# Optimization experiments

Measured on AMD Instinct MI355X. Metric: run time of the kernel, lower is better.

Reference implementation:

```python
import jax, jax.numpy as jnp
import numpy as np

L, H, NH, HD, F, B, S = 32, 1024, 16, 64, 2048, 2, 2048
HPH = H // NH  # hidden per attention head (hyena column split)
EPS = 1e-6
BLOCK = {0:'HCS',4:'HCS',7:'HCS',11:'HCS',14:'HCS',18:'HCS',21:'HCS',25:'HCS',28:'HCS',
         1:'HCM',5:'HCM',8:'HCM',12:'HCM',15:'HCM',19:'HCM',22:'HCM',26:'HCM',29:'HCM',
         2:'HCL',6:'HCL',9:'HCL',13:'HCL',16:'HCL',20:'HCL',23:'HCL',27:'HCL',30:'HCL',
         3:'ATT',10:'ATT',17:'ATT',24:'ATT',31:'ATT'}

def rmsnorm(x, w):
    return x * jax.lax.rsqrt(jnp.mean(x * x, -1, keepdims=True) + EPS) * w

def step_fir(u, state, w, b, flip=False, gated=False):
    # u:[B,C]  state:[B,C,cache]  w:[C,Lf]  b:[C]  (single-token FIR step)
    cache = state.shape[-1]
    w = w[:, ::-1][:, -(cache + 1):] if flip else w[:, :cache + 1]
    y = w[:, -1] * u + jnp.sum(state * w[:, :-1], -1)
    y = y + (b * u if gated else b)
    return y

def split3(z):
    # column_split_hyena=True path of _interleave_split
    r = z.reshape(z.shape[0], NH, 3 * HPH)
    x2 = r[:, :, :HPH].reshape(z.shape[0], H)
    x1 = r[:, :, HPH:2 * HPH].reshape(z.shape[0], H)
    v = r[:, :, 2 * HPH:].reshape(z.shape[0], H)
    return x2, x1, v

def mlp(x, W1, W2):
    return jax.nn.gelu(x @ W1.T) @ W2.T

def fir_block(x, n1, n2, pW, pb, oW, ob, W1, W2, sfw, sfb, h, D, fstate, istate, flip, gated):
    xn = rmsnorm(x, n1)
    z = xn @ pW.T + pb                 # [B,1,3H]
    u = z[:, -1]                       # [B,3H]
    zp = step_fir(u, fstate, sfw, sfb)
    x2, x1, v = split3(zp)
    y = step_fir(x1 * v, istate, h, D, flip=flip, gated=gated)
    y = (y * x2)[:, None]              # [B,1,H]
    x = y @ oW.T + ob + x
    return mlp(rmsnorm(x, n2), W1, W2) + x

def hcl_block(x, n1, n2, pW, pb, oW, ob, W1, W2, sfw, sfb, log_poles, residues, D, fstate, iir):
    xn = rmsnorm(x, n1)
    z = xn @ pW.T + pb
    u = z[:, -1]
    zp = step_fir(u, fstate, sfw, sfb)
    x2, x1, v = split3(zp)
    x1v = x1 * v
    iir_new = jnp.exp(log_poles) * iir + x1v[..., None]   # [B,H,SS] single-step IIR update
    res = jnp.sum(residues * iir_new, -1)
    y = (x2 * (res + D * x1v))[:, None]
    x = y @ oW.T + ob + x
    return mlp(rmsnorm(x, n2), W1, W2) + x

def att_block(x, n1, n2, qW, qb, oW, ob, W1, W2, kc, vc, cos, sin, pos):
    xn = rmsnorm(x, n1)
    qkv = (xn @ qW.T + qb).reshape(B, 1, 3, NH, HD)
    q, k, v = qkv[:, :, 0], qkv[:, :, 1], qkv[:, :, 2]
    c = jnp.concatenate([cos[pos], cos[pos]])  # [HD]
    s = jnp.concatenate([sin[pos], sin[pos]])
    rot = lambda t: jnp.concatenate([-t[..., HD // 2:], t[..., :HD // 2]], -1)
    q = q * c + rot(q) * s
    k = k * c + rot(k) * s
    kc = kc.at[:, pos].set(k[:, 0])  # KV-cache scatter write at current position
    vc = vc.at[:, pos].set(v[:, 0])
    scores = jnp.einsum('bohd,bshd->bhos', q, kc) * (HD ** -0.5)
    scores = jnp.where(jnp.arange(S) > pos, -10000.0, scores)
    aw = jax.nn.softmax(scores, -1)
    ctx = jnp.einsum('bhos,bshd->bohd', aw, vc).reshape(B, 1, H)
    x = ctx @ oW.T + ob + x
    return mlp(rmsnorm(x, n2), W1, W2) + x

def forward(x, position, norm1_w, norm2_w, proj_W, proj_b, out_W, out_b, mlp_W1, mlp_W2,
            sf_w, sf_b, hcs_h, hcs_D, hcm_h, hcm_D, hcl_logpoles, hcl_residues, hcl_D,
            fir_state, hcs_state, hcm_state, iir_state, k_cache, v_cache, rope_cos, rope_sin):
    att = 0
    for i in range(L):  # loop over 32 structurally distinct layers (static)
        t = BLOCK[i]
        cm = (norm1_w[i], norm2_w[i], proj_W[i], proj_b[i], out_W[i], out_b[i], mlp_W1[i], mlp_W2[i])
        if t == 'HCS':
            x = fir_block(x, *cm, sf_w[i], sf_b[i], hcs_h[i], hcs_D[i], fir_state[i], hcs_state[i], False, False)
        elif t == 'HCM':
            x = fir_block(x, *cm, sf_w[i], sf_b[i], hcm_h[i], hcm_D[i], fir_state[i], hcm_state[i], True, True)
        elif t == 'HCL':
            x = hcl_block(x, *cm, sf_w[i], sf_b[i], hcl_logpoles[i], hcl_residues[i], hcl_D[i], fir_state[i], iir_state[i])
        else:
            x = att_block(x, *cm, k_cache[att], v_cache[att], rope_cos, rope_sin, position)
            att += 1
    return x

def setup_inputs():
    key = jax.random.key(0)
    ks = jax.random.split(key, 24)
    g = lambda k, shape, sc: jax.random.normal(k, shape, jnp.float32) * sc
    inv_freq = 1.0 / (10000.0 ** (np.arange(0, HD, 2, dtype=np.float32) / HD))
    ang = np.arange(S, dtype=np.float32)[:, None] * inv_freq[None, :]
    return {
        'x': g(ks[0], (B, 1, H), 1.0),
        'position': 1024,
        'norm1_w': jnp.ones((L, H), jnp.float32),
        'norm2_w': jnp.ones((L, H), jnp.float32),
        'proj_W': g(ks[1], (L, 3 * H, H), H ** -0.5),
        'proj_b': jnp.zeros((L, 3 * H), jnp.float32),
        'out_W': g(ks[2], (L, H, H), 0.2 * H ** -0.5),
        'out_b': jnp.zeros((L, H), jnp.float32),
        'mlp_W1': g(ks[3], (L, F, H), H ** -0.5),
        'mlp_W2': g(ks[4], (L, H, F), 0.2 * F ** -0.5),
        'sf_w': g(ks[5], (L, 3 * H, 3), 0.4),
        'sf_b': g(ks[6], (L, 3 * H), 0.02),
        'hcs_h': g(ks[7], (L, H, 7), 0.2),
        'hcs_D': g(ks[8], (L, H), 0.2),
        'hcm_h': g(ks[9], (L, H, 128), 0.04),
        'hcm_D': g(ks[10], (L, H), 0.2),
        'hcl_logpoles': -jax.random.uniform(ks[11], (L, H, 16), jnp.float32, 0.01, 2.0),
        'hcl_residues': g(ks[12], (L, H, 16), 0.1),
        'hcl_D': g(ks[13], (L, H), 0.2),
        'fir_state': g(ks[14], (L, B, 3 * H, 2), 0.5),
        'hcs_state': g(ks[15], (L, B, H, 6), 0.5),
        'hcm_state': g(ks[16], (L, B, H, 127), 0.5),
        'iir_state': g(ks[17], (L, B, H, 16), 0.5),
        'k_cache': g(ks[18], (5, B, S, NH, HD), 1.0),
        'v_cache': g(ks[19], (5, B, S, NH, HD), 1.0),
        'rope_cos': jnp.asarray(np.cos(ang)),
        'rope_sin': jnp.asarray(np.sin(ang)),
    }

def reference(x, position, norm1_w, norm2_w, proj_W, proj_b, out_W, out_b, mlp_W1, mlp_W2,
              sf_w, sf_b, hcs_h, hcs_D, hcm_h, hcm_D, hcl_logpoles, hcl_residues, hcl_D,
              fir_state, hcs_state, hcm_state, iir_state, k_cache, v_cache, rope_cos, rope_sin):
    return forward(x, position, norm1_w, norm2_w, proj_W, proj_b, out_W, out_b, mlp_W1, mlp_W2,
                   sf_w, sf_b, hcs_h, hcs_D, hcm_h, hcm_D, hcl_logpoles, hcl_residues, hcl_D,
                   fir_state, hcs_state, hcm_state, iir_state, k_cache, v_cache, rope_cos, rope_sin)
```

## Files before the change

### kernel.cpp

```cpp
#include <hip/hip_runtime.h>
#include <hip/hip_bf16.h>
#include <math.h>

#define LAYERS 32
#define H      1024
#define H3     3072
#define NHEADS 16
#define HDIM   64
#define FF     2048
#define BATCH  2
#define SEQ    2048
#define EPSF   1e-6f

__device__ __forceinline__ float wredSum(float v) {
#pragma unroll
  for (int m = 32; m >= 1; m >>= 1) v += __shfl_xor(v, m, 64);
  return v;
}
__device__ __forceinline__ float wredMax(float v) {
#pragma unroll
  for (int m = 32; m >= 1; m >>= 1) v = fmaxf(v, __shfl_xor(v, m, 64));
  return v;
}
__device__ __forceinline__ float gelu_t(float x) {
  return 0.5f * x * (1.0f + tanhf(0.7978845608028654f * (x + 0.044715f * x * x * x)));
}

__global__ __launch_bounds__(256) void prep_kernel(
    const float* __restrict__ sf_w, const float* __restrict__ sf_b,
    const float* __restrict__ fir_state,
    const float* __restrict__ hcs_h, const float* __restrict__ hcs_D, const float* __restrict__ hcs_state,
    const float* __restrict__ hcm_h, const float* __restrict__ hcm_D, const float* __restrict__ hcm_state,
    const float* __restrict__ lp, const float* __restrict__ resd, const float* __restrict__ hcl_D,
    const float* __restrict__ iir,
    unsigned long long kbits,
    float* __restrict__ sfd, float* __restrict__ sfc,
    float* __restrict__ mix0, float* __restrict__ mix1)
{
  int blk = blockIdx.x, tid = threadIdx.x;
  if (blk < 768) {
    int idx = blk * 256 + tid;
    int i = idx / (BATCH * H3);
    int r = idx % (BATCH * H3);
    int b = r / H3, ch = r % H3;
    const float* fs = fir_state + ((size_t)(i * BATCH + b) * H3 + ch) * 2;
    const float* sw = sf_w + ((size_t)i * H3 + ch) * 3;
    sfd[idx] = fs[0] * sw[0] + fs[1] * sw[1] + sf_b[i * H3 + ch];
    if (b == 0) sfc[i * H3 + ch] = sw[2];
  } else if (blk < 1024) {
    int idx = (blk - 768) * 256 + tid;
    int i = idx >> 11;
    int r = idx & 2047;
    int b = r >> 10, c = r & 1023;
    int kind = (int)((kbits >> (2 * i)) & 3ull);
    if (kind == 0) {
      const float* st = hcs_state + ((size_t)(i * BATCH + b) * H + c) * 6;
      const float* hh = hcs_h + ((size_t)i * H + c) * 7;
      float acc = 0.f;
#pragma unroll
      for (int k = 0; k < 6; k++) acc += st[k] * hh[k];
      mix0[idx] = acc + hcs_D[i * H + c];
      if (b == 0) mix1[i * H + c] = hh[6];
    } else if (kind == 2) {
      const float* ii = iir + ((size_t)(i * BATCH + b) * H + c) * 16;
      const float* lpp = lp + ((size_t)i * H + c) * 16;
      const float* rs = resd + ((size_t)i * H + c) * 16;
      float acc = 0.f, rsum = 0.f;
#pragma unroll
      for (int k = 0; k < 16; k++) { float rv = rs[k]; acc += rv * expf(lpp[k]) * ii[k]; rsum += rv; }
      mix0[idx] = acc;
      if (b == 0) mix1[i * H + c] = rsum + hcl_D[i * H + c];
    }
  } else {
    int w = tid >> 6, lane = tid & 63;
    int widx = (blk - 1024) * 4 + w;
    if (widx < 9 * BATCH * H) {
      int li = widx >> 11;
      int r = widx & 2047;
      int b = r >> 10, c = r & 1023;
      int i = (li >> 1) * 7 + ((li & 1) ? 5 : 1);
      const float* st = hcm_state + ((size_t)(i * BATCH + b) * H + c) * 127;
      const float* hh = hcm_h + ((size_t)i * H + c) * 128;
      float acc = 0.f;
      int k = lane;
      if (k < 127) acc += st[k] * hh[127 - k];
      k = lane + 64;
      if (k < 127) acc += st[k] * hh[127 - k];
      acc = wredSum(acc);
      if (lane == 0) {
        mix0[(i * BATCH + b) * H + c] = acc;
        if (b == 0) mix1[i * H + c] = hh[0] + hcm_D[i * H + c];
      }
    }
  }
}

template<int ROWS, bool GELU, bool HASBIAS>
__global__ __launch_bounds__(256) void gemv_norm_kernel(
    const float* __restrict__ x, const float* __restrict__ nw,
    const float* __restrict__ W, const float* __restrict__ bias,
    float* __restrict__ out)
{
  __shared__ alignas(16) float xe[BATCH][H];
  __shared__ float red[8];
  __shared__ float scl[BATCH];
  int tid = threadIdx.x, lane = tid & 63, w = tid >> 6;
  int r0 = blockIdx.x * 8 + w * 2;
  const float4* row0 = (const float4*)(W + (size_t)r0 * H);
  const float4* row1 = (const float4*)(W + (size_t)(r0 + 1) * H);
  float4 wa[4], wb[4];
#pragma unroll
  for (int j = 0; j < 4; j++) { wa[j] = row0[lane + 64 * j]; wb[j] = row1[lane + 64 * j]; }

  float ss0 = 0.f, ss1 = 0.f;
#pragma unroll
  for (int it = 0; it < 8; it++) {
    int e = tid + it * 256;
    int b = e >> 10, c = e & 1023;
    float xv = x[b * H + c];
    xe[b][c] = xv * nw[c];
    if (it < 4) ss0 += xv * xv; else ss1 += xv * xv;
  }
  ss0 = wredSum(ss0); ss1 = wredSum(ss1);
  if (lane == 0) { red[w] = ss0; red[4 + w] = ss1; }
  __syncthreads();
  if (tid == 0) {
    scl[0] = rsqrtf((red[0] + red[1] + red[2] + red[3]) * (1.0f / H) + EPSF);
    scl[1] = rsqrtf((red[4] + red[5] + red[6] + red[7]) * (1.0f / H) + EPSF);
  }
  __syncthreads();

  float a00 = 0.f, a01 = 0.f, a10 = 0.f, a11 = 0.f;
  const float4* x0 = (const float4*)xe[0];
  const float4* x1 = (const float4*)xe[1];
#pragma unroll
  for (int j = 0; j < 4; j++) {
    float4 h0 = x0[lane + 64 * j], h1 = x1[lane + 64 * j];
    a00 += wa[j].x * h0.x + wa[j].y * h0.y + wa[j].z * h0.z + wa[j].w * h0.w;
    a01 += wa[j].x * h1.x + wa[j].y * h1.y + wa[j].z * h1.z + wa[j].w * h1.w;
    a10 += wb[j].x * h0.x + wb[j].y * h0.y + wb[j].z * h0.z + wb[j].w * h0.w;
    a11 += wb[j].x * h1.x + wb[j].y * h1.y + wb[j].z * h1.z + wb[j].w * h1.w;
  }
  a00 = wredSum(a00); a01 = wredSum(a01); a10 = wredSum(a10); a11 = wredSum(a11);
  if (lane == 0) {
    float s0 = scl[0], s1 = scl[1];
    float b0 = HASBIAS ? bias[r0] : 0.f;
    float b1 = HASBIAS ? bias[r0 + 1] : 0.f;
    float v00 = a00 * s0 + b0, v01 = a01 * s1 + b0;
    float v10 = a10 * s0 + b1, v11 = a11 * s1 + b1;
    if (GELU) { v00 = gelu_t(v00); v01 = gelu_t(v01); v10 = gelu_t(v10); v11 = gelu_t(v11); }
    out[0 * ROWS + r0] = v00;
    out[1 * ROWS + r0] = v01;
    out[0 * ROWS + r0 + 1] = v10;
    out[1 * ROWS + r0 + 1] = v11;
  }
}

__global__ __launch_bounds__(256) void mix_out_kernel(
    int kind,
    const float* __restrict__ z, const float* __restrict__ sfdL, const float* __restrict__ sfcL,
    const float* __restrict__ mix0L, const float* __restrict__ mix1L,
    const float* __restrict__ attP,
    const float* __restrict__ oW, const float* __restrict__ ob,
    const float* __restrict__ x_in, float* __restrict__ x_out)
{
  __shared__ alignas(16) float y[BATCH][H];
  int tid = threadIdx.x, lane = tid & 63, w = tid >> 6;
  int r0 = blockIdx.x * 8 + w * 2;
  const float4* row0 = (const float4*)(oW + (size_t)r0 * H);
  const float4* row1 = (const float4*)(oW + (size_t)(r0 + 1) * H);
  float4 wa[4], wb[4];
#pragma unroll
  for (int j = 0; j < 4; j++) { wa[j] = row0[lane + 64 * j]; wb[j] = row1[lane + 64 * j]; }

  if (kind < 3) {
#pragma unroll
    for (int it = 0; it < 8; it++) {
      int e = tid + it * 256;
      int b = e >> 10, c = e & 1023;
      int n = c >> 6, d = c & 63;
      int base = n * 192 + d;
      float x2 = sfcL[base] * z[b * H3 + base] + sfdL[b * H3 + base];
      float x1 = sfcL[base + 64] * z[b * H3 + base + 64] + sfdL[b * H3 + base + 64];
      float vv = sfcL[base + 128] * z[b * H3 + base + 128] + sfdL[b * H3 + base + 128];
      float t = x1 * vv;
      y[b][c] = (mix1L[c] * t + mix0L[b * H + c]) * x2;
    }
  } else {
#pragma unroll
    for (int it = 0; it < 8; it++) {
      int e = tid + it * 256;
      int b = e >> 10, c = e & 1023;
      int n = c >> 6, d = c & 63;
      float M = -1e30f;
#pragma unroll
      for (int sp = 0; sp < 8; sp++) M = fmaxf(M, attP[((sp * BATCH + b) * NHEADS + n) * 66 + 64]);
      float Ls = 0.f, num = 0.f;
#pragma unroll
      for (int sp = 0; sp < 8; sp++) {
        const float* P = attP + ((sp * BATCH + b) * NHEADS + n) * 66;
        float wgt = expf(P[64] - M);
        Ls += wgt * P[65];
        num += wgt * P[d];
      }
      y[b][c] = num / Ls;
    }
  }
  __syncthreads();

  float a00 = 0.f, a01 = 0.f, a10 = 0.f, a11 = 0.f;
  const float4* y0 = (const float4*)y[0];
  const float4* y1 = (const float4*)y[1];
#pragma unroll
  for (int j = 0; j < 4; j++) {
    float4 h0 = y0[lane + 64 * j], h1 = y1[lane + 64 * j];
    a00 += wa[j].x * h0.x + wa[j].y * h0.y + wa[j].z * h0.z + wa[j].w * h0.w;
    a01 += wa[j].x * h1.x + wa[j].y * h1.y + wa[j].z * h1.z + wa[j].w * h1.w;
    a10 += wb[j].x * h0.x + wb[j].y * h0.y + wb[j].z * h0.z + wb[j].w * h0.w;
    a11 += wb[j].x * h1.x + wb[j].y * h1.y + wb[j].z * h1.z + wb[j].w * h1.w;
  }
  a00 = wredSum(a00); a01 = wredSum(a01); a10 = wredSum(a10); a11 = wredSum(a11);
  if (lane == 0) {
    x_out[0 * H + r0]     = a00 + ob[r0]     + x_in[0 * H + r0];
    x_out[1 * H + r0]     = a01 + ob[r0]     + x_in[1 * H + r0];
    x_out[0 * H + r0 + 1] = a10 + ob[r0 + 1] + x_in[0 * H + r0 + 1];
    x_out[1 * H + r0 + 1] = a11 + ob[r0 + 1] + x_in[1 * H + r0 + 1];
  }
}

__global__ __launch_bounds__(256) void gemv_mlp2_kernel(
    const float* __restrict__ h, const float* __restrict__ W2,
    const float* __restrict__ x_in, float* __restrict__ x_out)
{
  __shared__ alignas(16) float hs[BATCH][FF];
  int tid = threadIdx.x, lane = tid & 63, w = tid >> 6;
  int r = blockIdx.x * 4 + w;
  const float4* row = (const float4*)(W2 + (size_t)r * FF);
  float4 wv[8];
#pragma unroll
  for (int j = 0; j < 8; j++) wv[j] = row[lane + 64 * j];
#pragma unroll
  for (int it = 0; it < 16; it++) {
    int e = tid + it * 256;
    int b = e >> 11, c = e & 2047;
    hs[b][c] = h[b * FF + c];
  }
  __syncthreads();
  float a0 = 0.f, a1 = 0.f;
  const float4* h0 = (const float4*)hs[0];
  const float4* h1 = (const float4*)hs[1];
#pragma unroll
  for (int j = 0; j < 8; j++) {
    float4 p = h0[lane + 64 * j], q = h1[lane + 64 * j];
    a0 += wv[j].x * p.x + wv[j].y * p.y + wv[j].z * p.z + wv[j].w * p.w;
    a1 += wv[j].x * q.x + wv[j].y * q.y + wv[j].z * q.z + wv[j].w * q.w;
  }
  a0 = wredSum(a0); a1 = wredSum(a1);
  if (lane == 0) {
    x_out[0 * H + r] = a0 + x_in[0 * H + r];
    x_out[1 * H + r] = a1 + x_in[1 * H + r];
  }
}

__global__ __launch_bounds__(256) void attn_kernel(
    const float* __restrict__ z, const int* __restrict__ posp,
    const float* __restrict__ kc, const float* __restrict__ vc,
    const float* __restrict__ cosT, const float* __restrict__ sinT,
    float* __restrict__ P)
{
  int sp = blockIdx.x & 7, n = (blockIdx.x >> 3) & 15, b = blockIdx.x >> 7;
  int pos = *posp;
  __shared__ alignas(16) float q_s[HDIM], k_s[HDIM], v_s[HDIM];
  __shared__ float eg[256];
  __shared__ float redA[4];
  __shared__ alignas(16) float osum[4][HDIM];
  int tid = threadIdx.x, lane = tid & 63, w = tid >> 6;

  if (tid < 64) {
    int d = tid, j = d & 31;
    float cs = cosT[pos * 32 + j], sn = sinT[pos * 32 + j];
    float qv = z[b * H3 + n * 64 + d];
    float qo = z[b * H3 + n * 64 + ((d + 32) & 63)];
    q_s[d] = ((d < 32) ? (qv * cs - qo * sn) : (qv * cs + qo * sn)) * 0.125f;
    float kv = z[b * H3 + 1024 + n * 64 + d];
    float ko = z[b * H3 + 1024 + n * 64 + ((d + 32) & 63)];
    k_s[d] = (d < 32) ? (kv * cs - ko * sn) : (kv * cs + ko * sn);
    v_s[d] = z[b * H3 + 2048 + n * 64 + d];
  }
  __syncthreads();

  int s = sp * 256 + tid;
  float logit = -1e30f;
  if (s <= pos) {
    const float4* k4 = (s == pos) ? (const float4*)k_s
                                  : (const float4*)(kc + (((size_t)b * SEQ + s) * NHEADS + n) * HDIM);
    const float4* q4 = (const float4*)q_s;
    float acc = 0.f;
#pragma unroll
    for (int j = 0; j < 16; j++) {
      float4 kk = k4[j], qq = q4[j];
      acc += kk.x * qq.x + kk.y * qq.y + kk.z * qq.z + kk.w * qq.w;
    }
    logit = acc;
  }
  float m = wredMax(logit);
  if (lane == 0) redA[w] = m;
  __syncthreads();
  m = fmaxf(fmaxf(redA[0], redA[1]), fmaxf(redA[2], redA[3]));
  float e = (s <= pos) ? expf(logit - m) : 0.f;
  eg[tid] = e;
  float ps = wredSum(e);
  __syncthreads();
  if (lane == 0) redA[w] = ps;
  __syncthreads();
  float lsum = redA[0] + redA[1] + redA[2] + redA[3];

  int dgrp = lane & 15, srow = lane >> 4;
  float4 acc = make_float4(0.f, 0.f, 0.f, 0.f);
#pragma unroll 4
  for (int it = 0; it < 16; it++) {
    int sl = w * 64 + it * 4;
    if (sp * 256 + sl > pos) break;
    int sli = sl + srow;
    int ss = sp * 256 + sli;
    float ev = eg[sli];
    const float4* v4 = (ss == pos) ? (const float4*)v_s
                                   : (const float4*)(vc + (((size_t)b * SEQ + ss) * NHEADS + n) * HDIM);
    float4 vv = v4[dgrp];
    acc.x += ev * vv.x; acc.y += ev * vv.y; acc.z += ev * vv.z; acc.w += ev * vv.w;
  }
#pragma unroll
  for (int mm = 16; mm <= 32; mm <<= 1) {
    acc.x += __shfl_xor(acc.x, mm, 64);
    acc.y += __shfl_xor(acc.y, mm, 64);
    acc.z += __shfl_xor(acc.z, mm, 64);
    acc.w += __shfl_xor(acc.w, mm, 64);
  }
  if (srow == 0) ((float4*)osum[w])[dgrp] = acc;
  __syncthreads();
  float* Pp = P + ((size_t)(sp * BATCH + b) * NHEADS + n) * 66;
  if (tid < 64) Pp[tid] = osum[0][tid] + osum[1][tid] + osum[2][tid] + osum[3][tid];
  if (tid == 64) Pp[64] = m;
  if (tid == 65) Pp[65] = lsum;
}

extern "C" void kernel_launch(void* const* d_in, const int* in_sizes, int n_in,
                              void* d_out, int out_size, void* d_ws, size_t ws_size,
                              hipStream_t stream) {
  (void)in_sizes; (void)n_in; (void)out_size; (void)ws_size;
  const float* x0    = (const float*)d_in[0];
  const int*   posp  = (const int*)d_in[1];
  const float* n1    = (const float*)d_in[2];
  const float* n2    = (const float*)d_in[3];
  const float* pW    = (const float*)d_in[4];
  const float* pb    = (const float*)d_in[5];
  const float* oW    = (const float*)d_in[6];
  const float* ob    = (const float*)d_in[7];
  const float* W1    = (const float*)d_in[8];
  const float* W2    = (const float*)d_in[9];
  const float* sfw   = (const float*)d_in[10];
  const float* sfb   = (const float*)d_in[11];
  const float* hcs_h = (const float*)d_in[12];
  const float* hcs_D = (const float*)d_in[13];
  const float* hcm_h = (const float*)d_in[14];
  const float* hcm_D = (const float*)d_in[15];
  const float* lp    = (const float*)d_in[16];
  const float* resd  = (const float*)d_in[17];
  const float* hclD  = (const float*)d_in[18];
  const float* fir   = (const float*)d_in[19];
  const float* hcsS  = (const float*)d_in[20];
  const float* hcmS  = (const float*)d_in[21];
  const float* iir   = (const float*)d_in[22];
  const float* kc    = (const float*)d_in[23];
  const float* vc    = (const float*)d_in[24];
  const float* cosT  = (const float*)d_in[25];
  const float* sinT  = (const float*)d_in[26];

  float* ws    = (float*)d_ws;
  float* xbuf0 = ws;
  float* xbuf1 = ws + 2048;
  float* zbuf  = ws + 4096;
  float* hbuf  = ws + 10240;
  float* attP  = ws + 14336;
  float* sfd   = ws + 31232;
  float* sfc   = ws + 227840;
  float* mix0  = ws + 326144;
  float* mix1  = ws + 391680;

  static const int KIND[LAYERS] = {0,1,2,3,0,1,2,0,1,2,3,0,1,2,0,1,2,3,0,1,2,0,1,2,3,0,1,2,0,1,2,3};
  unsigned long long kbits = 0ull;
  for (int i = 0; i < LAYERS; i++) kbits |= ((unsigned long long)KIND[i]) << (2 * i);

  prep_kernel<<<5632, 256, 0, stream>>>(sfw, sfb, fir, hcs_h, hcs_D, hcsS,
      hcm_h, hcm_D, hcmS, lp, resd, hclD, iir, kbits, sfd, sfc, mix0, mix1);

  const float* xsrc = x0;
  int att = 0;
  for (int i = 0; i < LAYERS; i++) {
    gemv_norm_kernel<H3, false, true><<<H3 / 8, 256, 0, stream>>>(
        xsrc, n1 + i * H, pW + (size_t)i * H3 * H, pb + i * H3, zbuf);
    if (KIND[i] == 3) {
      attn_kernel<<<256, 256, 0, stream>>>(
          zbuf, posp, kc + (size_t)att * BATCH * SEQ * NHEADS * HDIM,
          vc + (size_t)att * BATCH * SEQ * NHEADS * HDIM, cosT, sinT, attP);
      att++;
    }
    mix_out_kernel<<<H / 8, 256, 0, stream>>>(
        KIND[i], zbuf, sfd + (size_t)i * BATCH * H3, sfc + (size_t)i * H3,
        mix0 + (size_t)i * BATCH * H, mix1 + (size_t)i * H, attP,
        oW + (size_t)i * H * H, ob + i * H, xsrc, xbuf1);
    gemv_norm_kernel<FF, true, false><<<FF / 8, 256, 0, stream>>>(
        xbuf1, n2 + i * H, W1 + (size_t)i * FF * H, nullptr, hbuf);
    gemv_mlp2_kernel<<<H / 4, 256, 0, stream>>>(
        hbuf, W2 + (size_t)i * H * FF, xbuf1, (i == 31) ? (float*)d_out : xbuf0);
    xsrc = xbuf0;
  }
}
```

Measured before the change: 702.8 us.

## Fuse MLP up/down GEMVs with fixed-point atomic accumulation of residual

Merges the W1 GEMV+GELU and the W2 GEMV into one kernel. Each block computes 16 hidden units and scatters their W2 contribution into a 64-bit fixed-point accumulator with atomic adds, which keeps the sum deterministic. The next layer's projection and output kernels rebuild the residual stream from the accumulator plus the saved mid-layer activation, and a final small kernel writes the output. This removes one launch per layer and the intermediate hidden buffer round trip. The cost is strided W2 reads, global 64-bit atomics, and fixed-point quantization of the MLP output.

```diff
diff --git a/kernel.cpp b/kernel.cpp
--- a/kernel.cpp
+++ b/kernel.cpp
@@ -11,6 +11,8 @@
 #define BATCH  2
 #define SEQ    2048
 #define EPSF   1e-6f
+#define SCALE_D   17592186044416.0
+#define INV_SCALE 5.684341886080802e-14
 
 __device__ __forceinline__ float wredSum(float v) {
 #pragma unroll
@@ -24,6 +26,11 @@
 }
 __device__ __forceinline__ float gelu_t(float x) {
   return 0.5f * x * (1.0f + tanhf(0.7978845608028654f * (x + 0.044715f * x * x * x)));
+}
+__device__ __forceinline__ float combineX(const unsigned long long* accP, const float* xMP,
+                                          const float* x0f, int first, int e) {
+  if (first) return x0f[e];
+  return (float)((double)(long long)accP[e] * INV_SCALE) + xMP[e];
 }
 
 __global__ __launch_bounds__(256) void prep_kernel(
@@ -95,16 +102,18 @@
   }
 }
 
-template<int ROWS, bool GELU, bool HASBIAS>
-__global__ __launch_bounds__(256) void gemv_norm_kernel(
-    const float* __restrict__ x, const float* __restrict__ nw,
-    const float* __restrict__ W, const float* __restrict__ bias,
-    float* __restrict__ out)
+__global__ __launch_bounds__(256) void gemv_P(
+    const unsigned long long* __restrict__ accP, const float* __restrict__ xMP,
+    const float* __restrict__ x0f, int first,
+    const float* __restrict__ nw, const float* __restrict__ W,
+    const float* __restrict__ bias, float* __restrict__ out,
+    unsigned long long* __restrict__ accZ)
 {
   __shared__ alignas(16) float xe[BATCH][H];
   __shared__ float red[8];
   __shared__ float scl[BATCH];
   int tid = threadIdx.x, lane = tid & 63, w = tid >> 6;
+  if (blockIdx.x < 8) accZ[blockIdx.x * 256 + tid] = 0ull;
   int r0 = blockIdx.x * 8 + w * 2;
   const float4* row0 = (const float4*)(W + (size_t)r0 * H);
   const float4* row1 = (const float4*)(W + (size_t)(r0 + 1) * H);
@@ -117,7 +126,7 @@
   for (int it = 0; it < 8; it++) {
     int e = tid + it * 256;
     int b = e >> 10, c = e & 1023;
-    float xv = x[b * H + c];
+    float xv = combineX(accP, xMP, x0f, first, e);
     xe[b][c] = xv * nw[c];
     if (it < 4) ss0 += xv * xv; else ss1 += xv * xv;
   }
@@ -131,11 +140,11 @@
   __syncthreads();
 
   float a00 = 0.f, a01 = 0.f, a10 = 0.f, a11 = 0.f;
-  const float4* x0 = (const float4*)xe[0];
-  const float4* x1 = (const float4*)xe[1];
+  const float4* x0v = (const float4*)xe[0];
+  const float4* x1v = (const float4*)xe[1];
 #pragma unroll
   for (int j = 0; j < 4; j++) {
-    float4 h0 = x0[lane + 64 * j], h1 = x1[lane + 64 * j];
+    float4 h0 = x0v[lane + 64 * j], h1 = x1v[lane + 64 * j];
     a00 += wa[j].x * h0.x + wa[j].y * h0.y + wa[j].z * h0.z + wa[j].w * h0.w;
     a01 += wa[j].x * h1.x + wa[j].y * h1.y + wa[j].z * h1.z + wa[j].w * h1.w;
     a10 += wb[j].x * h0.x + wb[j].y * h0.y + wb[j].z * h0.z + wb[j].w * h0.w;
@@ -144,15 +153,11 @@
   a00 = wredSum(a00); a01 = wredSum(a01); a10 = wredSum(a10); a11 = wredSum(a11);
   if (lane == 0) {
     float s0 = scl[0], s1 = scl[1];
-    float b0 = HASBIAS ? bias[r0] : 0.f;
-    float b1 = HASBIAS ? bias[r0 + 1] : 0.f;
-    float v00 = a00 * s0 + b0, v01 = a01 * s1 + b0;
-    float v10 = a10 * s0 + b1, v11 = a11 * s1 + b1;
-    if (GELU) { v00 = gelu_t(v00); v01 = gelu_t(v01); v10 = gelu_t(v10); v11 = gelu_t(v11); }
-    out[0 * ROWS + r0] = v00;
-    out[1 * ROWS + r0] = v01;
-    out[0 * ROWS + r0 + 1] = v10;
-    out[1 * ROWS + r0 + 1] = v11;
+    float b0 = bias[r0], b1 = bias[r0 + 1];
+    out[0 * H3 + r0]     = a00 * s0 + b0;
+    out[1 * H3 + r0]     = a01 * s1 + b0;
+    out[0 * H3 + r0 + 1] = a10 * s0 + b1;
+    out[1 * H3 + r0 + 1] = a11 * s1 + b1;
   }
 }
 
@@ -162,7 +167,9 @@
     const float* __restrict__ mix0L, const float* __restrict__ mix1L,
     const float* __restrict__ attP,
     const float* __restrict__ oW, const float* __restrict__ ob,
-    const float* __restrict__ x_in, float* __restrict__ x_out)
+    const unsigned long long* __restrict__ accP, const float* __restrict__ xMP,
+    const float* __restrict__ x0f, int first,
+    float* __restrict__ x_out)
 {
   __shared__ alignas(16) float y[BATCH][H];
   int tid = threadIdx.x, lane = tid & 63, w = tid >> 6;
@@ -221,44 +228,89 @@
   }
   a00 = wredSum(a00); a01 = wredSum(a01); a10 = wredSum(a10); a11 = wredSum(a11);
   if (lane == 0) {
-    x_out[0 * H + r0]     = a00 + ob[r0]     + x_in[0 * H + r0];
-    x_out[1 * H + r0]     = a01 + ob[r0]     + x_in[1 * H + r0];
-    x_out[0 * H + r0 + 1] = a10 + ob[r0 + 1] + x_in[0 * H + r0 + 1];
-    x_out[1 * H + r0 + 1] = a11 + ob[r0 + 1] + x_in[1 * H + r0 + 1];
-  }
-}
-
-__global__ __launch_bounds__(256) void gemv_mlp2_kernel(
-    const float* __restrict__ h, const float* __restrict__ W2,
-    const float* __restrict__ x_in, float* __restrict__ x_out)
-{
-  __shared__ alignas(16) float hs[BATCH][FF];
+    x_out[0 * H + r0]     = a00 + ob[r0]     + combineX(accP, xMP, x0f, first, 0 * H + r0);
+    x_out[1 * H + r0]     = a01 + ob[r0]     + combineX(accP, xMP, x0f, first, 1 * H + r0);
+    x_out[0 * H + r0 + 1] = a10 + ob[r0 + 1] + combineX(accP, xMP, x0f, first, 0 * H + r0 + 1);
+    x_out[1 * H + r0 + 1] = a11 + ob[r0 + 1] + combineX(accP, xMP, x0f, first, 1 * H + r0 + 1);
+  }
+}
+
+__global__ __launch_bounds__(256) void mlp_fused(
+    const float* __restrict__ xM, const float* __restrict__ nw,
+    const float* __restrict__ W1, const float* __restrict__ W2,
+    unsigned long long* __restrict__ acc)
+{
+  __shared__ alignas(16) float xe[BATCH][H];
+  __shared__ float red[8];
+  __shared__ float scl[BATCH];
+  __shared__ float gh[BATCH][16];
   int tid = threadIdx.x, lane = tid & 63, w = tid >> 6;
-  int r = blockIdx.x * 4 + w;
-  const float4* row = (const float4*)(W2 + (size_t)r * FF);
-  float4 wv[8];
-#pragma unroll
-  for (int j = 0; j < 8; j++) wv[j] = row[lane + 64 * j];
-#pragma unroll
+  int f0 = blockIdx.x * 16;
+
+  float ss0 = 0.f, ss1 = 0.f;
+#pragma unroll
+  for (int it = 0; it < 8; it++) {
+    int e = tid + it * 256;
+    int b = e >> 10, c = e & 1023;
+    float xv = xM[e];
+    xe[b][c] = xv * nw[c];
+    if (it < 4) ss0 += xv * xv; else ss1 += xv * xv;
+  }
+  ss0 = wredSum(ss0); ss1 = wredSum(ss1);
+  if (lane == 0) { red[w] = ss0; red[4 + w] = ss1; }
+  __syncthreads();
+  if (tid == 0) {
+    scl[0] = rsqrtf((red[0] + red[1] + red[2] + red[3]) * (1.0f / H) + EPSF);
+    scl[1] = rsqrtf((red[4] + red[5] + red[6] + red[7]) * (1.0f / H) + EPSF);
+  }
+  __syncthreads();
+
+#pragma unroll
+  for (int p = 0; p < 2; p++) {
+    int fr = p * 8 + w * 2;
+    const float4* row0 = (const float4*)(W1 + (size_t)(f0 + fr) * H);
+    const float4* row1 = (const float4*)(W1 + (size_t)(f0 + fr + 1) * H);
+    float4 wa[4], wb[4];
+#pragma unroll
+    for (int j = 0; j < 4; j++) { wa[j] = row0[lane + 64 * j]; wb[j] = row1[lane + 64 * j]; }
+    float a00 = 0.f, a01 = 0.f, a10 = 0.f, a11 = 0.f;
+    const float4* x0v = (const float4*)xe[0];
+    const float4* x1v = (const float4*)xe[1];
+#pragma unroll
+    for (int j = 0; j < 4; j++) {
+      float4 h0 = x0v[lane + 64 * j], h1 = x1v[lane + 64 * j];
+      a00 += wa[j].x * h0.x + wa[j].y * h0.y + wa[j].z * h0.z + wa[j].w * h0.w;
+      a01 += wa[j].x * h1.x + wa[j].y * h1.y + wa[j].z * h1.z + wa[j].w * h1.w;
+      a10 += wb[j].x * h0.x + wb[j].y * h0.y + wb[j].z * h0.z + wb[j].w * h0.w;
+      a11 += wb[j].x * h1.x + wb[j].y * h1.y + wb[j].z * h1.z + wb[j].w * h1.w;
+    }
+    a00 = wredSum(a00); a01 = wredSum(a01); a10 = wredSum(a10); a11 = wredSum(a11);
+    if (lane == 0) {
+      gh[0][fr]     = gelu_t(a00 * scl[0]);
+      gh[1][fr]     = gelu_t(a01 * scl[1]);
+      gh[0][fr + 1] = gelu_t(a10 * scl[0]);
+      gh[1][fr + 1] = gelu_t(a11 * scl[1]);
+    }
+  }
+  __syncthreads();
+
+  int q = tid >> 2, part = tid & 3;
+  float g00 = gh[0][part * 4 + 0], g01 = gh[0][part * 4 + 1],
+        g02 = gh[0][part * 4 + 2], g03 = gh[0][part * 4 + 3];
+  float g10 = gh[1][part * 4 + 0], g11 = gh[1][part * 4 + 1],
+        g12 = gh[1][part * 4 + 2], g13 = gh[1][part * 4 + 3];
+#pragma unroll 4
   for (int it = 0; it < 16; it++) {
-    int e = tid + it * 256;
-    int b = e >> 11, c = e & 2047;
-    hs[b][c] = h[b * FF + c];
-  }
-  __syncthreads();
-  float a0 = 0.f, a1 = 0.f;
-  const float4* h0 = (const float4*)hs[0];
-  const float4* h1 = (const float4*)hs[1];
-#pragma unroll
-  for (int j = 0; j < 8; j++) {
-    float4 p = h0[lane + 64 * j], q = h1[lane + 64 * j];
-    a0 += wv[j].x * p.x + wv[j].y * p.y + wv[j].z * p.z + wv[j].w * p.w;
-    a1 += wv[j].x * q.x + wv[j].y * q.y + wv[j].z * q.z + wv[j].w * q.w;
-  }
-  a0 = wredSum(a0); a1 = wredSum(a1);
-  if (lane == 0) {
-    x_out[0 * H + r] = a0 + x_in[0 * H + r];
-    x_out[1 * H + r] = a1 + x_in[1 * H + r];
+    int r = it * 64 + q;
+    float4 wv = *(const float4*)(W2 + (size_t)r * FF + f0 + part * 4);
+    float d0 = wv.x * g00 + wv.y * g01 + wv.z * g02 + wv.w * g03;
+    float d1 = wv.x * g10 + wv.y * g11 + wv.z * g12 + wv.w * g13;
+    d0 += __shfl_xor(d0, 1, 64); d0 += __shfl_xor(d0, 2, 64);
+    d1 += __shfl_xor(d1, 1, 64); d1 += __shfl_xor(d1, 2, 64);
+    if (part == 0) {
+      atomicAdd(&acc[r],        (unsigned long long)(long long)llrint((double)d0 * SCALE_D));
+      atomicAdd(&acc[H + r],    (unsigned long long)(long long)llrint((double)d1 * SCALE_D));
+    }
   }
 }
 
@@ -342,6 +394,14 @@
   if (tid < 64) Pp[tid] = osum[0][tid] + osum[1][tid] + osum[2][tid] + osum[3][tid];
   if (tid == 64) Pp[64] = m;
   if (tid == 65) Pp[65] = lsum;
+}
+
+__global__ __launch_bounds__(256) void finalize_k(
+    const unsigned long long* __restrict__ acc, const float* __restrict__ xM,
+    float* __restrict__ out)
+{
+  int e = blockIdx.x * 256 + threadIdx.x;
+  out[e] = (float)((double)(long long)acc[e] * INV_SCALE) + xM[e];
 }
 
 extern "C" void kernel_launch(void* const* d_in, const int* in_sizes, int n_in,
@@ -377,15 +437,16 @@
   const float* sinT  = (const float*)d_in[26];
 
   float* ws    = (float*)d_ws;
-  float* xbuf0 = ws;
-  float* xbuf1 = ws + 2048;
-  float* zbuf  = ws + 4096;
-  float* hbuf  = ws + 10240;
-  float* attP  = ws + 14336;
-  float* sfd   = ws + 31232;
-  float* sfc   = ws + 227840;
-  float* mix0  = ws + 326144;
-  float* mix1  = ws + 391680;
+  float* zbuf  = ws;
+  float* attP  = ws + 6144;
+  float* xM0   = ws + 23040;
+  float* xM1   = ws + 25088;
+  unsigned long long* acc0 = (unsigned long long*)(ws + 27136);
+  unsigned long long* acc1 = (unsigned long long*)(ws + 31232);
+  float* sfd   = ws + 35328;
+  float* sfc   = ws + 231936;
+  float* mix0  = ws + 330240;
+  float* mix1  = ws + 395776;
 
   static const int KIND[LAYERS] = {0,1,2,3,0,1,2,0,1,2,3,0,1,2,0,1,2,3,0,1,2,0,1,2,3,0,1,2,0,1,2,3};
   unsigned long long kbits = 0ull;
@@ -394,11 +455,14 @@
   prep_kernel<<<5632, 256, 0, stream>>>(sfw, sfb, fir, hcs_h, hcs_D, hcsS,
       hcm_h, hcm_D, hcmS, lp, resd, hclD, iir, kbits, sfd, sfc, mix0, mix1);
 
-  const float* xsrc = x0;
-  int att = 0;
+  const unsigned long long* accP = nullptr;
+  const float* xMP = nullptr;
+  int first = 1, att = 0;
   for (int i = 0; i < LAYERS; i++) {
-    gemv_norm_kernel<H3, false, true><<<H3 / 8, 256, 0, stream>>>(
-        xsrc, n1 + i * H, pW + (size_t)i * H3 * H, pb + i * H3, zbuf);
+    unsigned long long* accW = (i & 1) ? acc1 : acc0;
+    float* xMW = (i & 1) ? xM1 : xM0;
+    gemv_P<<<H3 / 8, 256, 0, stream>>>(
+        accP, xMP, x0, first, n1 + i * H, pW + (size_t)i * H3 * H, pb + i * H3, zbuf, accW);
     if (KIND[i] == 3) {
       attn_kernel<<<256, 256, 0, stream>>>(
           zbuf, posp, kc + (size_t)att * BATCH * SEQ * NHEADS * HDIM,
@@ -408,11 +472,10 @@
     mix_out_kernel<<<H / 8, 256, 0, stream>>>(
         KIND[i], zbuf, sfd + (size_t)i * BATCH * H3, sfc + (size_t)i * H3,
         mix0 + (size_t)i * BATCH * H, mix1 + (size_t)i * H, attP,
-        oW + (size_t)i * H * H, ob + i * H, xsrc, xbuf1);
-    gemv_norm_kernel<FF, true, false><<<FF / 8, 256, 0, stream>>>(
-        xbuf1, n2 + i * H, W1 + (size_t)i * FF * H, nullptr, hbuf);
-    gemv_mlp2_kernel<<<H / 4, 256, 0, stream>>>(
-        hbuf, W2 + (size_t)i * H * FF, xbuf1, (i == 31) ? (float*)d_out : xbuf0);
-    xsrc = xbuf0;
-  }
-}
+        oW + (size_t)i * H * H, ob + i * H, accP, xMP, x0, first, xMW);
+    mlp_fused<<<FF / 16, 256, 0, stream>>>(
+        xMW, n2 + i * H, W1 + (size_t)i * FF * H, W2 + (size_t)i * H * FF, accW);
+    accP = accW; xMP = xMW; first = 0;
+  }
+  finalize_k<<<8, 256, 0, stream>>>(acc1, xM1, (float*)d_out);
+}
```

After: 1.178 ms. 67.7% more time.
